# Kernel optimization log

Hardware: AMD Instinct MI355X
Metric: run time of the kernel (lower is better)

The kernel has to match this reference:

```python
import jax, jax.numpy as jnp
import numpy as np

V = 29       # alphabet size (len(IN_LOOKUP))
H = 1024     # hidden_size
L = 4        # layers
B = 64       # batch
S = 512      # seq len


def setup_inputs() -> dict:
    key = jax.random.key(0)
    ks = jax.random.split(key, 8)
    padded_in = jax.random.randint(ks[0], (B, S), 0, V)
    # pack-style per-timestep active batch sizes: non-increasing, in [1, B]
    in_lengths = jnp.sort(jax.random.randint(ks[1], (S,), 1, B + 1))[::-1]
    emb = jax.random.normal(ks[2], (V, H), jnp.float32)
    scale = 1.0 / np.sqrt(H)
    w_ih = jax.random.uniform(ks[3], (L, 4 * H, H), jnp.float32, -scale, scale)
    w_hh = jax.random.uniform(ks[4], (L, 4 * H, H), jnp.float32, -scale, scale)
    b_ih = jax.random.uniform(ks[5], (L, 4 * H), jnp.float32, -scale, scale)
    b_hh = jax.random.uniform(ks[6], (L, 4 * H), jnp.float32, -scale, scale)
    return {"padded_in": padded_in, "in_lengths": in_lengths, "emb": emb,
            "w_ih": w_ih, "w_hh": w_hh, "b_ih": b_ih, "b_hh": b_hh}


def _lstm_cell(y, h, c, wi, wh, bi, bh):
    # PyTorch LSTMCell gate order: i, f, g, o
    gates = y @ wi.T + bi + h @ wh.T + bh          # [b, 4H]
    i, f, g, o = jnp.split(gates, 4, axis=-1)
    c_new = jax.nn.sigmoid(f) * c + jax.nn.sigmoid(i) * jnp.tanh(g)
    h_new = jax.nn.sigmoid(o) * jnp.tanh(c_new)
    return h_new, c_new


def reference(padded_in, in_lengths, emb, w_ih, w_hh, b_ih, b_hh):
    Bn, Sn = padded_in.shape
    Ln = w_ih.shape[0]
    Hn = emb.shape[1]
    emb = emb.at[0].set(0.0)                       # padding_idx=0 row is zero
    x = emb[padded_in]                             # [B, S, H]
    xs = (jnp.swapaxes(x, 0, 1), in_lengths)       # ([S, B, H], [S])
    h0 = jnp.zeros((Ln, Bn, Hn), x.dtype)
    c0 = jnp.zeros((Ln, Bn, Hn), x.dtype)
    row = jnp.arange(Bn)[:, None]                  # [B, 1]

    def step(carry, inp):
        h, c = carry
        x_t, bs = inp
        mask = row < bs                            # active rows this timestep
        y = x_t
        hs, cs = [], []
        for l in range(Ln):
            h_new, c_new = _lstm_cell(y, h[l], c[l], w_ih[l], w_hh[l], b_ih[l], b_hh[l])
            hs.append(jnp.where(mask, h_new, h[l]))
            cs.append(jnp.where(mask, c_new, c[l]))
            y = jnp.where(mask, h_new + h[l], y)   # residual feed to next layer
        return (jnp.stack(hs), jnp.stack(cs)), None

    (h, c), _ = jax.lax.scan(step, (h0, c0), xs)
    return h[-1]                                   # [B, H]
```

## Files before the change

kernel.cpp:

```cpp
#include <hip/hip_runtime.h>
#include <hip/hip_fp16.h>

#define Vn 29
#define Hn 1024
#define Ln 4
#define Bn 64
#define Sn 512
#define BH (Bn * Hn)
#define NBLK 256

typedef _Float16 half8 __attribute__((ext_vector_type(8)));
typedef _Float16 half4v __attribute__((ext_vector_type(4)));
typedef float f32x16 __attribute__((ext_vector_type(16)));
typedef float f32x4 __attribute__((ext_vector_type(4)));

__device__ __forceinline__ float sigmf(float x) { return 1.0f / (1.0f + __expf(-x)); }
__device__ __forceinline__ float tanhf_(float x) { return 1.0f - 2.0f / (__expf(2.0f * x) + 1.0f); }

__device__ __forceinline__ int perm_off(int r, int j) {
    return (((j >> 4) * 2 + (r >> 5)) << 9) + ((((j >> 3) & 1) << 5) + (r & 31)) * 8 + (j & 7);
}

__device__ __forceinline__ half4v ldg_llc4(const _Float16* p) {
    half4v v;
    asm volatile("global_load_dwordx2 %0, %1, off sc0 sc1" : "=v"(v) : "v"(p) : "memory");
    return v;
}

__device__ __forceinline__ void gld_lds16(const _Float16* g, _Float16* l) {
    __builtin_amdgcn_global_load_lds(
        (const __attribute__((address_space(1))) void*)g,
        (__attribute__((address_space(3))) void*)l, 16, 0, 17);
}

__device__ __forceinline__ void stg_coh4(_Float16* p, half4v v) {
    union { half4v h; unsigned long long u; } c;
    c.h = v;
    __hip_atomic_store((unsigned long long*)p, c.u, __ATOMIC_RELAXED,
                       __HIP_MEMORY_SCOPE_AGENT);
}

#define BAR_INTS 320

__global__ void init_kernel(const float* __restrict__ bi, const float* __restrict__ bh,
                            const float* __restrict__ emb, int* __restrict__ bar,
                            float* __restrict__ biasf, _Float16* __restrict__ ehi,
                            _Float16* __restrict__ hbh) {
    int i = blockIdx.x * blockDim.x + threadIdx.x;
    int stride = gridDim.x * blockDim.x;
    for (int k = i; k < BAR_INTS; k += stride) bar[k] = 0;
    for (int k = i; k < Ln * 4 * Hn; k += stride) biasf[k] = bi[k] + bh[k];
    for (int k = i; k < Vn * Hn; k += stride)
        ehi[k] = (_Float16)((k < Hn) ? 0.f : emb[k]);
    for (int k = i; k < 2 * Ln * Bn * Hn; k += stride) hbh[k] = (_Float16)0.f;
}

__device__ __forceinline__ void grid_barrier(int* __restrict__ bar, int bid, int step) {
    asm volatile("s_waitcnt vmcnt(0)" ::: "memory");
    __syncthreads();
    if (threadIdx.x == 0) {
        int* c0 = bar + (bid & 7) * 32;
        int* c1 = bar + 256;
        int* gen = bar + 288;
        bool rel = false;
        int p = __hip_atomic_fetch_add(c0, 1, __ATOMIC_RELAXED, __HIP_MEMORY_SCOPE_AGENT);
        if (p == 32 * step - 1) {
            int q = __hip_atomic_fetch_add(c1, 1, __ATOMIC_RELAXED, __HIP_MEMORY_SCOPE_AGENT);
            if (q == 8 * step - 1) {
                __hip_atomic_store(gen, step, __ATOMIC_RELAXED, __HIP_MEMORY_SCOPE_AGENT);
                rel = true;
            }
        }
        if (!rel) {
            long long t0 = clock64();
            int it = 0;
            while (__hip_atomic_load(gen, __ATOMIC_RELAXED, __HIP_MEMORY_SCOPE_AGENT) < step) {
                __builtin_amdgcn_s_sleep(1);
                if (((++it) & 255) == 0 && clock64() - t0 > 2000000000LL) break;
            }
        }
    }
    __syncthreads();
}

template <int KS, int MT>
struct KStepL {
    static __device__ __forceinline__ void run(const _Float16* a0, const _Float16* a1,
                                               _Float16* s0, _Float16* s1,
                                               int lane, half8 (&x0)[2], half8 (&x1)[2],
                                               const half8 (&wf)[2][16],
                                               f32x16 (&acc)[MT][2]) {
        if constexpr (KS < 15) {
            constexpr int CNT = (14 - KS) < 8 ? (14 - KS) : 8;
            asm volatile("s_waitcnt vmcnt(%0)" :: "i"(MT * CNT) : "memory");
            constexpr int rs = (KS + 1 < 10) ? KS + 1 : KS - 9;
            x0[(KS + 1) & 1] = *reinterpret_cast<const half8*>(s0 + rs * 512 + lane * 8);
            if constexpr (MT == 2)
                x1[(KS + 1) & 1] = *reinterpret_cast<const half8*>(s1 + rs * 512 + lane * 8);
        }
        acc[0][0] = __builtin_amdgcn_mfma_f32_32x32x16_f16(x0[KS & 1], wf[0][KS], acc[0][0], 0, 0, 0);
        acc[0][1] = __builtin_amdgcn_mfma_f32_32x32x16_f16(x0[KS & 1], wf[1][KS], acc[0][1], 0, 0, 0);
        if constexpr (MT == 2) {
            acc[1][0] = __builtin_amdgcn_mfma_f32_32x32x16_f16(x1[KS & 1], wf[0][KS], acc[1][0], 0, 0, 0);
            acc[1][1] = __builtin_amdgcn_mfma_f32_32x32x16_f16(x1[KS & 1], wf[1][KS], acc[1][1], 0, 0, 0);
        }
        if constexpr (KS + 10 < 16) {
            gld_lds16(a0 + (KS + 10) * 1024, s0 + KS * 512);
            if constexpr (MT == 2) gld_lds16(a1 + (KS + 10) * 1024, s1 + KS * 512);
        }
        KStepL<KS + 1, MT>::run(a0, a1, s0, s1, lane, x0, x1, wf, acc);
    }
};
template <int MT>
struct KStepL<16, MT> {
    static __device__ __forceinline__ void run(const _Float16*, const _Float16*, _Float16*,
                                               _Float16*, int, half8 (&)[2], half8 (&)[2],
                                               const half8 (&)[2][16], f32x16 (&)[MT][2]) {}
};

template <int MT>
__device__ __forceinline__ void cell_compute_lds(const _Float16* a0, const _Float16* a1,
                                                 _Float16* s0, _Float16* s1, int lane,
                                                 const half8 (&wf)[2][16],
                                                 f32x16 (&acc)[MT][2]) {
#pragma unroll
    for (int mt = 0; mt < MT; ++mt)
#pragma unroll
        for (int nt = 0; nt < 2; ++nt)
#pragma unroll
            for (int r = 0; r < 16; ++r) acc[mt][nt][r] = 0.f;
#pragma unroll
    for (int i = 0; i < 10; ++i) {
        gld_lds16(a0 + i * 1024, s0 + i * 512);
        if constexpr (MT == 2) gld_lds16(a1 + i * 1024, s1 + i * 512);
    }
    asm volatile("s_waitcnt vmcnt(%0)" :: "i"(MT * 9) : "memory");
    half8 x0[2], x1[2];
    x0[0] = *reinterpret_cast<const half8*>(s0 + lane * 8);
    if constexpr (MT == 2) x1[0] = *reinterpret_cast<const half8*>(s1 + lane * 8);
    KStepL<0, MT>::run(a0, a1, s0, s1, lane, x0, x1, wf, acc);
}

template <int MT>
__device__ __forceinline__ void cell_compute_plain(const _Float16* __restrict__ a0,
                                                   const _Float16* __restrict__ a1,
                                                   const half8 (&wf)[2][16],
                                                   f32x16 (&acc)[MT][2]) {
#pragma unroll
    for (int mt = 0; mt < MT; ++mt)
#pragma unroll
        for (int nt = 0; nt < 2; ++nt)
#pragma unroll
            for (int r = 0; r < 16; ++r) acc[mt][nt][r] = 0.f;
#pragma unroll
    for (int ks = 0; ks < 16; ++ks) {
        half8 x0 = *reinterpret_cast<const half8*>(a0 + ks * 16);
        acc[0][0] = __builtin_amdgcn_mfma_f32_32x32x16_f16(x0, wf[0][ks], acc[0][0], 0, 0, 0);
        acc[0][1] = __builtin_amdgcn_mfma_f32_32x32x16_f16(x0, wf[1][ks], acc[0][1], 0, 0, 0);
        if constexpr (MT == 2) {
            half8 x1 = *reinterpret_cast<const half8*>(a1 + ks * 16);
            acc[1][0] = __builtin_amdgcn_mfma_f32_32x32x16_f16(x1, wf[0][ks], acc[1][0], 0, 0, 0);
            acc[1][1] = __builtin_amdgcn_mfma_f32_32x32x16_f16(x1, wf[1][ks], acc[1][1], 0, 0, 0);
        }
    }
}

template <int MT, bool ADD>
__device__ __forceinline__ void part_write(float (*pw)[64], const f32x16 (&acc)[MT][2],
                                           int lane) {
    const int ln = lane & 31;
#pragma unroll
    for (int mt = 0; mt < MT; ++mt)
#pragma unroll
        for (int nt = 0; nt < 2; ++nt)
#pragma unroll
            for (int r = 0; r < 16; ++r) {
                int m = mt * 32 + 4 * (lane >> 5) + (r & 3) + 8 * (r >> 2);
                int n = nt * 32 + ln;
                int idx = n ^ ((m & 7) << 2);
                if (ADD) pw[m][idx] += acc[mt][nt][r];
                else pw[m][idx] = acc[mt][nt][r];
            }
}

__global__ __launch_bounds__(512, 2) void lstm_persistent(
    const int* __restrict__ padded_in, const int* __restrict__ in_lengths,
    const float* __restrict__ w_ih, const float* __restrict__ w_hh,
    const float* __restrict__ biasf, int* __restrict__ bar,
    const _Float16* __restrict__ ehi, _Float16* __restrict__ hbh,
    _Float16* __restrict__ ybh, float* __restrict__ out) {
    __shared__ __align__(1024) char ldsbuf[163840];

    const int cu = blockIdx.x;
    const int layer = cu >> 6;
    const int j0 = (cu & 63) * 16;
    const int tid = threadIdx.x;
    const int wv = tid >> 6;
    const int lane = tid & 63;
    const int ln = lane & 31;
    const int khalf = (lane >> 5) * 8;
    const bool isH = (wv >= 4);
    const int kb = (isH ? (wv - 4) : wv) * 256;

    _Float16* s0 = reinterpret_cast<_Float16*>(ldsbuf) + wv * 10240;
    _Float16* s1 = s0 + 5120;

    half8 wf[2][16];
    {
        const float* wsrc = isH ? w_hh : w_ih;
#pragma unroll
        for (int nt = 0; nt < 2; ++nt) {
            int n = nt * 32 + ln;
            const float* rowp =
                wsrc + ((size_t)layer * 4 * Hn + (n >> 4) * Hn + j0 + (n & 15)) * Hn + kb + khalf;
#pragma unroll
            for (int ks = 0; ks < 16; ++ks) {
                f32x4 a = *reinterpret_cast<const f32x4*>(rowp + ks * 16);
                f32x4 b = *reinterpret_cast<const f32x4*>(rowp + ks * 16 + 4);
                half8 h;
                h[0] = (_Float16)a[0]; h[1] = (_Float16)a[1];
                h[2] = (_Float16)a[2]; h[3] = (_Float16)a[3];
                h[4] = (_Float16)b[0]; h[5] = (_Float16)b[1];
                h[6] = (_Float16)b[2]; h[7] = (_Float16)b[3];
                wf[nt][ks] = h;
            }
        }
    }

    const int brow = (tid & 255) >> 2;
    const int jcol = (tid & 3) * 4;
    const int J = j0 + jcol;
    const int po = perm_off(brow, J);
    float bias[4][4];
#pragma unroll
    for (int g = 0; g < 4; ++g)
#pragma unroll
        for (int p = 0; p < 4; ++p)
            bias[g][p] = biasf[layer * 4096 + g * 1024 + J + p];

    float creg[4] = {0.f, 0.f, 0.f, 0.f};
    float hreg[4] = {0.f, 0.f, 0.f, 0.f};

    const bool carryOwner = (tid < 256) && (layer > 0) && (layer < 3);

    for (int w = 0; w < Sn + Ln - 1; ++w) {
        const int t = w - layer;
        if (t >= 0 && t < Sn) {
            const int bs = in_lengths[t];
            const int pin = t & 1;
            const int pout = pin ^ 1;

            const int lim0 = bs < 32 ? bs : 32;
            const int lim1 = bs - 32;
            const int off0 = (ln < lim0) ? lane * 8 : (lane & 32) * 8;
            const int off1 = (ln < lim1) ? lane * 8 : (lane & 32) * 8;

            half4v ycarry{};
            if (carryOwner && brow >= bs)
                ycarry = ldg_llc4(&ybh[(size_t)(pin * 3 + layer - 1) * BH + po]);

            const _Float16 *a0, *a1;
            bool coh;
            if (!isH) {
                if (layer == 0) {
                    const int ko = kb + khalf;
                    a0 = ehi + (size_t)padded_in[ln * Sn + t] * Hn + ko;
                    a1 = ehi + (size_t)padded_in[(32 + ln) * Sn + t] * Hn + ko;
                    coh = false;
                } else {
                    const _Float16* cb =
                        ybh + (size_t)(pin * 3 + layer - 1) * BH + (size_t)kb * 64;
                    a0 = cb + off0;
                    a1 = cb + 512 + off1;
                    coh = true;
                }
            } else {
                const _Float16* cb =
                    hbh + (size_t)(pin * Ln + layer) * BH + (size_t)kb * 64;
                a0 = cb + off0;
                a1 = cb + 512 + off1;
                coh = true;
            }

            if (bs > 32) {
                f32x16 acc[2][2];
                if (coh) cell_compute_lds<2>(a0, a1, s0, s1, lane, wf, acc);
                else cell_compute_plain<2>(a0, a1, wf, acc);
                if (wv < 4)
                    part_write<2, false>(
                        reinterpret_cast<float (*)[64]>(ldsbuf + (size_t)wv * 20480), acc, lane);
                __syncthreads();
                if (wv >= 4)
                    part_write<2, true>(
                        reinterpret_cast<float (*)[64]>(ldsbuf + (size_t)(wv - 4) * 20480), acc,
                        lane);
            } else {
                f32x16 acc[1][2];
                if (coh) cell_compute_lds<1>(a0, a1, s0, s1, lane, wf, acc);
                else cell_compute_plain<1>(a0, a1, wf, acc);
                if (wv < 4)
                    part_write<1, false>(
                        reinterpret_cast<float (*)[64]>(ldsbuf + (size_t)wv * 20480), acc, lane);
                __syncthreads();
                if (wv >= 4)
                    part_write<1, true>(
                        reinterpret_cast<float (*)[64]>(ldsbuf + (size_t)(wv - 4) * 20480), acc,
                        lane);
            }
            __syncthreads();

            if (tid < 256) {
                float gsum[4][4];
#pragma unroll
                for (int g = 0; g < 4; ++g) {
                    int nidx = (g * 16 + jcol) ^ ((brow & 7) << 2);
                    const char* pb = ldsbuf + (size_t)brow * 256 + (size_t)nidx * 4;
                    f32x4 s = *reinterpret_cast<const f32x4*>(pb);
#pragma unroll
                    for (int p2 = 1; p2 < 4; ++p2)
                        s = s + *reinterpret_cast<const f32x4*>(pb + (size_t)p2 * 20480);
#pragma unroll
                    for (int p = 0; p < 4; ++p) gsum[g][p] = s[p] + bias[g][p];
                }

                const bool active = (brow < bs);
                float hold[4], ysum[4];
#pragma unroll
                for (int p = 0; p < 4; ++p) {
                    float cn = sigmf(gsum[1][p]) * creg[p] + sigmf(gsum[0][p]) * tanhf_(gsum[2][p]);
                    float hn = sigmf(gsum[3][p]) * tanhf_(cn);
                    hold[p] = hreg[p];
                    if (active) { creg[p] = cn; hreg[p] = hn; }
                    ysum[p] = hreg[p] + hold[p];
                }
                if (active) {
                    half4v hh;
#pragma unroll
                    for (int p = 0; p < 4; ++p) hh[p] = (_Float16)hreg[p];
                    stg_coh4(&hbh[(size_t)(pout * Ln + layer) * BH + po], hh);
                }
                if (layer < 3) {
                    half4v yh;
                    if (active) {
#pragma unroll
                        for (int p = 0; p < 4; ++p) yh[p] = (_Float16)ysum[p];
                    } else {
                        if (layer == 0) {
                            int ib = padded_in[brow * Sn + t];
                            yh = *reinterpret_cast<const half4v*>(&ehi[(size_t)ib * Hn + J]);
                        } else {
                            yh = ycarry;
                        }
                    }
                    stg_coh4(&ybh[(size_t)(pin * 3 + layer) * BH + po], yh);
                }
            }
        }
        grid_barrier(bar, cu, w + 1);
    }

    if (layer == 3 && tid < 256) {
        f32x4 o;
#pragma unroll
        for (int p = 0; p < 4; ++p) o[p] = hreg[p];
        *reinterpret_cast<f32x4*>(&out[(size_t)brow * Hn + J]) = o;
    }
}

extern "C" void kernel_launch(void* const* d_in, const int* in_sizes, int n_in,
                              void* d_out, int out_size, void* d_ws, size_t ws_size,
                              hipStream_t stream) {
    const int* padded_in = (const int*)d_in[0];
    const int* in_lengths = (const int*)d_in[1];
    const float* emb = (const float*)d_in[2];
    const float* w_ih = (const float*)d_in[3];
    const float* w_hh = (const float*)d_in[4];
    const float* b_ih = (const float*)d_in[5];
    const float* b_hh = (const float*)d_in[6];
    float* outp = (float*)d_out;

    char* w = (char*)d_ws;
    int* bar = (int*)w;            w += BAR_INTS * 4;
    float* biasf = (float*)w;      w += (size_t)Ln * 4 * Hn * 4;
    _Float16* ehi = (_Float16*)w;  w += (size_t)Vn * Hn * 2;
    _Float16* hbh = (_Float16*)w;  w += (size_t)2 * Ln * Bn * Hn * 2;
    _Float16* ybh = (_Float16*)w;  w += (size_t)2 * 3 * Bn * Hn * 2;

    init_kernel<<<256, 256, 0, stream>>>(b_ih, b_hh, emb, bar, biasf, ehi, hbh);
    lstm_persistent<<<NBLK, 512, 0, stream>>>(padded_in, in_lengths, w_ih, w_hh, biasf, bar,
                                              ehi, hbh, ybh, outp);
}
```

Baseline: 6.111 ms.

## Spread gate epilogue over all 512 threads and fully prefetch single-tile LDS path

The LSTM cell epilogue now uses all 512 threads, each handling 2 hidden columns instead of 4, where previously only 256 threads did this work. The coherent stores and loads shrink from 8 bytes to 4 bytes to match. In the MT==1 path, all 16 K-slices are now issued as global-to-LDS loads up front through a dedicated KStepF chain, instead of a 10-deep rolling prefetch. The aim is to shorten the serial per-timestep epilogue and the load latency on the recurrent critical path, at the cost of more, smaller memory transactions.

```diff
diff --git a/kernel.cpp b/kernel.cpp
--- a/kernel.cpp
+++ b/kernel.cpp
@@ -10,9 +10,9 @@
 #define NBLK 256
 
 typedef _Float16 half8 __attribute__((ext_vector_type(8)));
-typedef _Float16 half4v __attribute__((ext_vector_type(4)));
 typedef float f32x16 __attribute__((ext_vector_type(16)));
 typedef float f32x4 __attribute__((ext_vector_type(4)));
+typedef float f32x2 __attribute__((ext_vector_type(2)));
 
 __device__ __forceinline__ float sigmf(float x) { return 1.0f / (1.0f + __expf(-x)); }
 __device__ __forceinline__ float tanhf_(float x) { return 1.0f - 2.0f / (__expf(2.0f * x) + 1.0f); }
@@ -21,9 +21,9 @@
     return (((j >> 4) * 2 + (r >> 5)) << 9) + ((((j >> 3) & 1) << 5) + (r & 31)) * 8 + (j & 7);
 }
 
-__device__ __forceinline__ half4v ldg_llc4(const _Float16* p) {
-    half4v v;
-    asm volatile("global_load_dwordx2 %0, %1, off sc0 sc1" : "=v"(v) : "v"(p) : "memory");
+__device__ __forceinline__ unsigned int ldg_llc2(const _Float16* p) {
+    unsigned int v;
+    asm volatile("global_load_dword %0, %1, off sc0 sc1" : "=v"(v) : "v"(p) : "memory");
     return v;
 }
 
@@ -33,11 +33,10 @@
         (__attribute__((address_space(3))) void*)l, 16, 0, 17);
 }
 
-__device__ __forceinline__ void stg_coh4(_Float16* p, half4v v) {
-    union { half4v h; unsigned long long u; } c;
-    c.h = v;
-    __hip_atomic_store((unsigned long long*)p, c.u, __ATOMIC_RELAXED,
-                       __HIP_MEMORY_SCOPE_AGENT);
+__device__ __forceinline__ void stg_coh2(_Float16* p, _Float16 a, _Float16 b) {
+    union { _Float16 h[2]; unsigned int u; } c;
+    c.h[0] = a; c.h[1] = b;
+    __hip_atomic_store((unsigned int*)p, c.u, __ATOMIC_RELAXED, __HIP_MEMORY_SCOPE_AGENT);
 }
 
 #define BAR_INTS 320
@@ -83,39 +82,55 @@
     __syncthreads();
 }
 
-template <int KS, int MT>
+template <int KS>
 struct KStepL {
     static __device__ __forceinline__ void run(const _Float16* a0, const _Float16* a1,
                                                _Float16* s0, _Float16* s1,
                                                int lane, half8 (&x0)[2], half8 (&x1)[2],
                                                const half8 (&wf)[2][16],
-                                               f32x16 (&acc)[MT][2]) {
+                                               f32x16 (&acc)[2][2]) {
         if constexpr (KS < 15) {
             constexpr int CNT = (14 - KS) < 8 ? (14 - KS) : 8;
-            asm volatile("s_waitcnt vmcnt(%0)" :: "i"(MT * CNT) : "memory");
+            asm volatile("s_waitcnt vmcnt(%0)" :: "i"(2 * CNT) : "memory");
             constexpr int rs = (KS + 1 < 10) ? KS + 1 : KS - 9;
             x0[(KS + 1) & 1] = *reinterpret_cast<const half8*>(s0 + rs * 512 + lane * 8);
-            if constexpr (MT == 2)
-                x1[(KS + 1) & 1] = *reinterpret_cast<const half8*>(s1 + rs * 512 + lane * 8);
+            x1[(KS + 1) & 1] = *reinterpret_cast<const half8*>(s1 + rs * 512 + lane * 8);
         }
         acc[0][0] = __builtin_amdgcn_mfma_f32_32x32x16_f16(x0[KS & 1], wf[0][KS], acc[0][0], 0, 0, 0);
         acc[0][1] = __builtin_amdgcn_mfma_f32_32x32x16_f16(x0[KS & 1], wf[1][KS], acc[0][1], 0, 0, 0);
-        if constexpr (MT == 2) {
-            acc[1][0] = __builtin_amdgcn_mfma_f32_32x32x16_f16(x1[KS & 1], wf[0][KS], acc[1][0], 0, 0, 0);
-            acc[1][1] = __builtin_amdgcn_mfma_f32_32x32x16_f16(x1[KS & 1], wf[1][KS], acc[1][1], 0, 0, 0);
-        }
+        acc[1][0] = __builtin_amdgcn_mfma_f32_32x32x16_f16(x1[KS & 1], wf[0][KS], acc[1][0], 0, 0, 0);
+        acc[1][1] = __builtin_amdgcn_mfma_f32_32x32x16_f16(x1[KS & 1], wf[1][KS], acc[1][1], 0, 0, 0);
         if constexpr (KS + 10 < 16) {
             gld_lds16(a0 + (KS + 10) * 1024, s0 + KS * 512);
-            if constexpr (MT == 2) gld_lds16(a1 + (KS + 10) * 1024, s1 + KS * 512);
-        }
-        KStepL<KS + 1, MT>::run(a0, a1, s0, s1, lane, x0, x1, wf, acc);
+            gld_lds16(a1 + (KS + 10) * 1024, s1 + KS * 512);
+        }
+        KStepL<KS + 1>::run(a0, a1, s0, s1, lane, x0, x1, wf, acc);
     }
 };
-template <int MT>
-struct KStepL<16, MT> {
+template <>
+struct KStepL<16> {
     static __device__ __forceinline__ void run(const _Float16*, const _Float16*, _Float16*,
                                                _Float16*, int, half8 (&)[2], half8 (&)[2],
-                                               const half8 (&)[2][16], f32x16 (&)[MT][2]) {}
+                                               const half8 (&)[2][16], f32x16 (&)[2][2]) {}
+};
+
+template <int KS>
+struct KStepF {
+    static __device__ __forceinline__ void run(_Float16* s0, int lane, half8 (&x0)[2],
+                                               const half8 (&wf)[2][16], f32x16 (&acc)[1][2]) {
+        if constexpr (KS < 15) {
+            asm volatile("s_waitcnt vmcnt(%0)" :: "i"(14 - KS) : "memory");
+            x0[(KS + 1) & 1] = *reinterpret_cast<const half8*>(s0 + (KS + 1) * 512 + lane * 8);
+        }
+        acc[0][0] = __builtin_amdgcn_mfma_f32_32x32x16_f16(x0[KS & 1], wf[0][KS], acc[0][0], 0, 0, 0);
+        acc[0][1] = __builtin_amdgcn_mfma_f32_32x32x16_f16(x0[KS & 1], wf[1][KS], acc[0][1], 0, 0, 0);
+        KStepF<KS + 1>::run(s0, lane, x0, wf, acc);
+    }
+};
+template <>
+struct KStepF<16> {
+    static __device__ __forceinline__ void run(_Float16*, int, half8 (&)[2],
+                                               const half8 (&)[2][16], f32x16 (&)[1][2]) {}
 };
 
 template <int MT>
@@ -129,16 +144,25 @@
         for (int nt = 0; nt < 2; ++nt)
 #pragma unroll
             for (int r = 0; r < 16; ++r) acc[mt][nt][r] = 0.f;
-#pragma unroll
-    for (int i = 0; i < 10; ++i) {
-        gld_lds16(a0 + i * 1024, s0 + i * 512);
-        if constexpr (MT == 2) gld_lds16(a1 + i * 1024, s1 + i * 512);
-    }
-    asm volatile("s_waitcnt vmcnt(%0)" :: "i"(MT * 9) : "memory");
-    half8 x0[2], x1[2];
-    x0[0] = *reinterpret_cast<const half8*>(s0 + lane * 8);
-    if constexpr (MT == 2) x1[0] = *reinterpret_cast<const half8*>(s1 + lane * 8);
-    KStepL<0, MT>::run(a0, a1, s0, s1, lane, x0, x1, wf, acc);
+    if constexpr (MT == 2) {
+#pragma unroll
+        for (int i = 0; i < 10; ++i) {
+            gld_lds16(a0 + i * 1024, s0 + i * 512);
+            gld_lds16(a1 + i * 1024, s1 + i * 512);
+        }
+        asm volatile("s_waitcnt vmcnt(18)" ::: "memory");
+        half8 x0[2], x1[2];
+        x0[0] = *reinterpret_cast<const half8*>(s0 + lane * 8);
+        x1[0] = *reinterpret_cast<const half8*>(s1 + lane * 8);
+        KStepL<0>::run(a0, a1, s0, s1, lane, x0, x1, wf, acc);
+    } else {
+#pragma unroll
+        for (int i = 0; i < 16; ++i) gld_lds16(a0 + i * 1024, s0 + i * 512);
+        asm volatile("s_waitcnt vmcnt(15)" ::: "memory");
+        half8 x0[2];
+        x0[0] = *reinterpret_cast<const half8*>(s0 + lane * 8);
+        KStepF<0>::run(s0, lane, x0, wf, acc);
+    }
 }
 
 template <int MT>
@@ -227,21 +251,21 @@
         }
     }
 
-    const int brow = (tid & 255) >> 2;
-    const int jcol = (tid & 3) * 4;
+    const int brow = tid >> 3;
+    const int jcol = (tid & 7) * 2;
     const int J = j0 + jcol;
     const int po = perm_off(brow, J);
-    float bias[4][4];
+    float bias[4][2];
 #pragma unroll
     for (int g = 0; g < 4; ++g)
 #pragma unroll
-        for (int p = 0; p < 4; ++p)
+        for (int p = 0; p < 2; ++p)
             bias[g][p] = biasf[layer * 4096 + g * 1024 + J + p];
 
-    float creg[4] = {0.f, 0.f, 0.f, 0.f};
-    float hreg[4] = {0.f, 0.f, 0.f, 0.f};
-
-    const bool carryOwner = (tid < 256) && (layer > 0) && (layer < 3);
+    float creg[2] = {0.f, 0.f};
+    float hreg[2] = {0.f, 0.f};
+
+    const bool carryOwner = (layer > 0) && (layer < 3);
 
     for (int w = 0; w < Sn + Ln - 1; ++w) {
         const int t = w - layer;
@@ -255,9 +279,9 @@
             const int off0 = (ln < lim0) ? lane * 8 : (lane & 32) * 8;
             const int off1 = (ln < lim1) ? lane * 8 : (lane & 32) * 8;
 
-            half4v ycarry{};
+            unsigned int ycarry = 0;
             if (carryOwner && brow >= bs)
-                ycarry = ldg_llc4(&ybh[(size_t)(pin * 3 + layer - 1) * BH + po]);
+                ycarry = ldg_llc2(&ybh[(size_t)(pin * 3 + layer - 1) * BH + po]);
 
             const _Float16 *a0, *a1;
             bool coh;
@@ -309,24 +333,24 @@
             }
             __syncthreads();
 
-            if (tid < 256) {
-                float gsum[4][4];
+            {
+                float gsum[4][2];
 #pragma unroll
                 for (int g = 0; g < 4; ++g) {
                     int nidx = (g * 16 + jcol) ^ ((brow & 7) << 2);
                     const char* pb = ldsbuf + (size_t)brow * 256 + (size_t)nidx * 4;
-                    f32x4 s = *reinterpret_cast<const f32x4*>(pb);
+                    f32x2 s = *reinterpret_cast<const f32x2*>(pb);
 #pragma unroll
                     for (int p2 = 1; p2 < 4; ++p2)
-                        s = s + *reinterpret_cast<const f32x4*>(pb + (size_t)p2 * 20480);
-#pragma unroll
-                    for (int p = 0; p < 4; ++p) gsum[g][p] = s[p] + bias[g][p];
+                        s = s + *reinterpret_cast<const f32x2*>(pb + (size_t)p2 * 20480);
+#pragma unroll
+                    for (int p = 0; p < 2; ++p) gsum[g][p] = s[p] + bias[g][p];
                 }
 
                 const bool active = (brow < bs);
-                float hold[4], ysum[4];
-#pragma unroll
-                for (int p = 0; p < 4; ++p) {
+                float hold[2], ysum[2];
+#pragma unroll
+                for (int p = 0; p < 2; ++p) {
                     float cn = sigmf(gsum[1][p]) * creg[p] + sigmf(gsum[0][p]) * tanhf_(gsum[2][p]);
                     float hn = sigmf(gsum[3][p]) * tanhf_(cn);
                     hold[p] = hreg[p];
@@ -334,36 +358,36 @@
                     ysum[p] = hreg[p] + hold[p];
                 }
                 if (active) {
-                    half4v hh;
-#pragma unroll
-                    for (int p = 0; p < 4; ++p) hh[p] = (_Float16)hreg[p];
-                    stg_coh4(&hbh[(size_t)(pout * Ln + layer) * BH + po], hh);
+                    stg_coh2(&hbh[(size_t)(pout * Ln + layer) * BH + po],
+                             (_Float16)hreg[0], (_Float16)hreg[1]);
                 }
                 if (layer < 3) {
-                    half4v yh;
                     if (active) {
-#pragma unroll
-                        for (int p = 0; p < 4; ++p) yh[p] = (_Float16)ysum[p];
+                        stg_coh2(&ybh[(size_t)(pin * 3 + layer) * BH + po],
+                                 (_Float16)ysum[0], (_Float16)ysum[1]);
                     } else {
+                        unsigned int u;
                         if (layer == 0) {
                             int ib = padded_in[brow * Sn + t];
-                            yh = *reinterpret_cast<const half4v*>(&ehi[(size_t)ib * Hn + J]);
+                            u = *reinterpret_cast<const unsigned int*>(&ehi[(size_t)ib * Hn + J]);
                         } else {
-                            yh = ycarry;
+                            u = ycarry;
                         }
+                        __hip_atomic_store(
+                            (unsigned int*)&ybh[(size_t)(pin * 3 + layer) * BH + po], u,
+                            __ATOMIC_RELAXED, __HIP_MEMORY_SCOPE_AGENT);
                     }
-                    stg_coh4(&ybh[(size_t)(pin * 3 + layer) * BH + po], yh);
                 }
             }
         }
         grid_barrier(bar, cu, w + 1);
     }
 
-    if (layer == 3 && tid < 256) {
-        f32x4 o;
-#pragma unroll
-        for (int p = 0; p < 4; ++p) o[p] = hreg[p];
-        *reinterpret_cast<f32x4*>(&out[(size_t)brow * Hn + J]) = o;
+    if (layer == 3) {
+        f32x2 o;
+        o[0] = hreg[0];
+        o[1] = hreg[1];
+        *reinterpret_cast<f32x2*>(&out[(size_t)brow * Hn + J]) = o;
     }
 }
 
```

After: 5.727 ms. 1.07x faster.
